# Kernel tuning notes

Measured on AMD Instinct MI355X. Metric: run time of the kernel, lower is better.

The kernel has to match this reference:

```python
import jax, jax.numpy as jnp
import numpy as np

NUM_NODES = 100000
NUM_EDGES = 1600000
NUM_GRAPHS = 1000
NUM_FEATURES = 128
DIM = 32
NUM_CLASSES = 10


def setup_inputs() -> dict:
    key = jax.random.key(0)
    ks = jax.random.split(key, 20)
    inp = {
        "x": jax.random.normal(ks[0], (NUM_NODES, NUM_FEATURES), dtype=jnp.float32),
        "edge_index": jax.random.randint(ks[1], (2, NUM_EDGES), 0, NUM_NODES, dtype=jnp.int64),
        "batch": jnp.sort(jax.random.randint(ks[2], (NUM_NODES,), 0, NUM_GRAPHS, dtype=jnp.int64)),
        "edge_weight": jax.random.uniform(ks[3], (NUM_EDGES,), dtype=jnp.float32),
    }
    # GraphConv params: lin_rel (with bias) on aggregated msgs, lin_root (no bias) on x
    dims = [(NUM_FEATURES, DIM)] + [(DIM, DIM)] * 4
    for i, (fi, fo) in enumerate(dims, start=1):
        s = 1.0 / np.sqrt(fi)
        inp[f"Wrel{i}"] = jax.random.uniform(ks[3 + i], (fi, fo), jnp.float32, -s, s)
        inp[f"brel{i}"] = jax.random.uniform(ks[8 + i], (fo,), jnp.float32, -s, s)
        inp[f"Wroot{i}"] = jax.random.uniform(ks[13 + i], (fi, fo), jnp.float32, -s, s)
    s = 1.0 / np.sqrt(DIM)
    inp["Wlin1"] = jax.random.uniform(ks[19], (DIM, DIM), jnp.float32, -s, s)
    inp["blin1"] = jax.random.uniform(jax.random.fold_in(key, 100), (DIM,), jnp.float32, -s, s)
    inp["Wlin2"] = jax.random.uniform(jax.random.fold_in(key, 101), (DIM, NUM_CLASSES), jnp.float32, -s, s)
    inp["blin2"] = jax.random.uniform(jax.random.fold_in(key, 102), (NUM_CLASSES,), jnp.float32, -s, s)
    return inp


def _graph_conv(x, src, dst, ew, Wrel, brel, Wroot, num_nodes):
    # message: x_j * e_ji ; aggregate (add) at target ; out = lin_rel(agg) + lin_root(x)
    msg = x[src] * ew[:, None]                                   # [E, F_in]
    agg = jax.ops.segment_sum(msg, dst, num_segments=num_nodes)  # [N, F_in]
    return agg @ Wrel + brel + x @ Wroot


def reference(x, edge_index, batch, edge_weight,
              Wrel1, brel1, Wroot1, Wrel2, brel2, Wroot2,
              Wrel3, brel3, Wroot3, Wrel4, brel4, Wroot4,
              Wrel5, brel5, Wroot5, Wlin1, blin1, Wlin2, blin2):
    n = x.shape[0]
    src, dst = edge_index[0], edge_index[1]
    h = jax.nn.relu(_graph_conv(x, src, dst, edge_weight, Wrel1, brel1, Wroot1, n))
    h = jax.nn.relu(_graph_conv(h, src, dst, edge_weight, Wrel2, brel2, Wroot2, n))
    h = jax.nn.relu(_graph_conv(h, src, dst, edge_weight, Wrel3, brel3, Wroot3, n))
    h = jax.nn.relu(_graph_conv(h, src, dst, edge_weight, Wrel4, brel4, Wroot4, n))
    h = jax.nn.relu(_graph_conv(h, src, dst, edge_weight, Wrel5, brel5, Wroot5, n))
    g = jax.ops.segment_sum(h, batch, num_segments=NUM_GRAPHS)   # global_add_pool [G, DIM]
    g = jax.nn.relu(g @ Wlin1 + blin1)
    # dropout p=0.5 is identity in eval mode
    logits = g @ Wlin2 + blin2
    return jax.nn.log_softmax(logits, axis=-1)
```

## Files before the change

kernel.cpp:

```cpp
#include <hip/hip_runtime.h>
#include <stdint.h>

#define NN 100000
#define NE 1600000
#define NG 1000
#define FIN 128
#define DIM 32
#define NC 10

#define NBKT 512
#define NPB 196
#define BCAP 4608
#define RND 2048
#define CURS 16
#define NBINB 782
#define NMM1 1563
#define MM1P1 781
#define MM1P2 782
#define WP 36

typedef unsigned int u32;
typedef __attribute__((ext_vector_type(8))) short short8;
typedef __attribute__((ext_vector_type(4))) float floatx4;
typedef __attribute__((ext_vector_type(4))) unsigned int uint4e;

__device__ __forceinline__ ushort f2bf(float f) {
    u32 b = __float_as_uint(f);
    return (ushort)((b + 0x7FFFu + ((b >> 16) & 1u)) >> 16);
}
__device__ __forceinline__ float bf2f(ushort u) {
    return __uint_as_float(((u32)u) << 16);
}

union SMemU {
    struct {
        uint2  ent[RND];
        ushort bk16[RND];
        int cnt[NBKT]; int sA[NBKT]; int sB[NBKT]; int gbase[NBKT];
    } b;
    struct {
        uint2 ent[BCAP];
        int hist[NPB]; int sc[NPB]; int base[NPB];
    } c;
    struct {
        ushort xs[64 * 136];
        ushort wrel[FIN * WP];
        ushort wroot[FIN * WP];
    } m;
};

__global__ __launch_bounds__(256) void k_init(u32* __restrict__ zp, int zn,
        const float* __restrict__ W1r, const float* __restrict__ W1o,
        const float* __restrict__ W2r, const float* __restrict__ W2o,
        const float* __restrict__ W3r, const float* __restrict__ W3o,
        const float* __restrict__ W4r, const float* __restrict__ W4o,
        ushort* __restrict__ wfrag) {
    int i = blockIdx.x * 256 + threadIdx.x;
    if (i < zn) zp[i] = 0u;
    if (blockIdx.x < 4) {
        const float* Ws[8] = {W1r, W1o, W2r, W2o, W3r, W3o, W4r, W4o};
        int t = threadIdx.x;
        int mat  = t >> 7;
        int nh   = (t >> 6) & 1;
        int lane = t & 63;
        const float* W = Ws[blockIdx.x * 2 + mat];
        int m = lane & 15;
        int g = lane >> 4;
        ushort* dst = wfrag + (((size_t)blockIdx.x * 4 + mat * 2 + nh) * 64 + lane) * 8;
        #pragma unroll
        for (int j = 0; j < 8; ++j)
            dst[j] = f2bf(W[(g * 8 + j) * DIM + nh * 16 + m]);
    }
}

__device__ void bin_body(SMemU& sm, int blk, const int* __restrict__ ei,
        const float* __restrict__ ew, int* __restrict__ cursor,
        uint2* __restrict__ ebuf) {
    int tid = threadIdx.x;
    int e0 = blk * RND;
    int n  = min(RND, NE - e0);

    for (int i = tid; i < NBKT; i += 256) sm.b.cnt[i] = 0;
    __syncthreads();

    u32 pk[8], wv[8], bp[8];
    #pragma unroll
    for (int q = 0; q < 8; ++q) {
        int i = tid + q * 256;
        pk[q] = 0; wv[q] = 0; bp[q] = 0;
        if (i < n) {
            int s = ei[e0 + i];
            int d = ei[NE + e0 + i];
            float w = ew[e0 + i];
            int b = d / NPB;
            int loc = d - b * NPB;
            int p = atomicAdd(&sm.b.cnt[b], 1);
            pk[q] = (u32)s | ((u32)loc << 17);
            wv[q] = __float_as_uint(w);
            bp[q] = (u32)p | ((u32)b << 16);
        }
    }
    __syncthreads();

    for (int i = tid; i < NBKT; i += 256) sm.b.sA[i] = sm.b.cnt[i];
    __syncthreads();
    int* ssrc = sm.b.sA; int* sdst = sm.b.sB;
    for (int dd = 1; dd < NBKT; dd <<= 1) {
        for (int i = tid; i < NBKT; i += 256)
            sdst[i] = ssrc[i] + (i >= dd ? ssrc[i - dd] : 0);
        __syncthreads();
        int* t = ssrc; ssrc = sdst; sdst = t;
    }
    for (int i = tid; i < NBKT; i += 256) {
        int excl = ssrc[i] - sm.b.cnt[i];
        sdst[i] = excl;
        if (sm.b.cnt[i] > 0) sm.b.gbase[i] = atomicAdd(&cursor[i * CURS], sm.b.cnt[i]);
    }
    __syncthreads();
    int* basep = sdst;

    #pragma unroll
    for (int q = 0; q < 8; ++q) {
        int i = tid + q * 256;
        if (i < n) {
            int b = (int)(bp[q] >> 16);
            int p = (int)(bp[q] & 0xFFFFu);
            int pos = basep[b] + p;
            sm.b.ent[pos]  = make_uint2(pk[q], wv[q]);
            sm.b.bk16[pos] = (ushort)b;
        }
    }
    __syncthreads();

    for (int i = tid; i < n; i += 256) {
        int b = (int)sm.b.bk16[i];
        int dsti = sm.b.gbase[b] + (i - basep[b]);
        if (dsti < BCAP) ebuf[(size_t)b * BCAP + dsti] = sm.b.ent[i];
    }
}

__device__ void csr_body(SMemU& sm, int bkt, uint2* __restrict__ ebuf,
        const int* __restrict__ cursor, uint2* __restrict__ od) {
    int tid = threadIdx.x;
    int cnt = min(cursor[bkt * CURS], 4096);
    for (int i = tid; i < NPB; i += 256) sm.c.hist[i] = 0;
    __syncthreads();
    uint2* gb = ebuf + (size_t)bkt * BCAP;
    uint2 my[16]; int mp[16];
    #pragma unroll
    for (int q = 0; q < 16; ++q) {
        int i = tid + q * 256;
        mp[q] = -1;
        if (i < cnt) {
            my[q] = gb[i];
            int loc = (int)(my[q].x >> 17);
            mp[q] = atomicAdd(&sm.c.hist[loc], 1);
        }
    }
    __syncthreads();
    for (int i = tid; i < NPB; i += 256) sm.c.sc[i] = (sm.c.hist[i] + 7) & ~7;
    __syncthreads();
    for (int dd = 1; dd < NPB; dd <<= 1) {
        int v = 0;
        if (tid < NPB) { v = sm.c.sc[tid]; if (tid >= dd) v += sm.c.sc[tid - dd]; }
        __syncthreads();
        if (tid < NPB) sm.c.sc[tid] = v;
        __syncthreads();
    }
    for (int i = tid; i < NPB; i += 256) sm.c.base[i] = sm.c.sc[i] - ((sm.c.hist[i] + 7) & ~7);
    __syncthreads();
    int tot = min(sm.c.sc[NPB - 1], BCAP);
    for (int i = tid; i < tot; i += 256) sm.c.ent[i] = make_uint2(0u, 0u);
    __syncthreads();
    #pragma unroll
    for (int q = 0; q < 16; ++q) {
        if (mp[q] >= 0) {
            int loc = (int)(my[q].x >> 17);
            int pos = sm.c.base[loc] + mp[q];
            if (pos < BCAP) sm.c.ent[pos] = my[q];
        }
    }
    __syncthreads();
    for (int i = tid; i < tot; i += 256) gb[i] = sm.c.ent[i];
    for (int i = tid; i < NPB; i += 256) {
        int node = bkt * NPB + i;
        if (node < NN) {
            int dg = sm.c.hist[i];
            int bs = sm.c.base[i];
            if (bs + ((dg + 7) & ~7) > BCAP) dg = max(0, BCAP - bs) & ~7;
            od[node] = make_uint2((u32)(bkt * BCAP + bs), (u32)dg);
        }
    }
}

__device__ void mm1_body(SMemU& sm, int blk, const float* __restrict__ x,
        const float* __restrict__ Wrel, const float* __restrict__ brel,
        const float* __restrict__ Wroot,
        ushort* __restrict__ ybf, float* __restrict__ aggi) {
    int tid = threadIdx.x;
    int base = blk * 64;
    for (int i = tid; i < FIN * DIM / 4; i += 256) {
        int k = i >> 3, c = i & 7;
        float4 v1 = ((const float4*)Wrel)[i];
        float4 v2 = ((const float4*)Wroot)[i];
        ushort4 u1, u2;
        u1.x = f2bf(v1.x); u1.y = f2bf(v1.y); u1.z = f2bf(v1.z); u1.w = f2bf(v1.w);
        u2.x = f2bf(v2.x); u2.y = f2bf(v2.y); u2.z = f2bf(v2.z); u2.w = f2bf(v2.w);
        *(ushort4*)&sm.m.wrel[k * WP + c * 4]  = u1;
        *(ushort4*)&sm.m.wroot[k * WP + c * 4] = u2;
    }
    for (int i = tid; i < 64 * 32; i += 256) {
        int r = i >> 5, c = i & 31;
        int node = base + r;
        float4 v = make_float4(0.f, 0.f, 0.f, 0.f);
        if (node < NN) v = ((const float4*)x)[(size_t)node * 32 + c];
        ushort4 u;
        u.x = f2bf(v.x); u.y = f2bf(v.y); u.z = f2bf(v.z); u.w = f2bf(v.w);
        *(ushort4*)&sm.m.xs[r * 136 + c * 4] = u;
    }
    __syncthreads();
    int lane = tid & 63;
    int w = tid >> 6;
    int m = lane & 15;
    int q = lane >> 4;
    short8 bfr[4][4];
    #pragma unroll
    for (int nt = 0; nt < 4; ++nt) {
        const ushort* W = (nt < 2) ? sm.m.wrel : sm.m.wroot;
        int ncol = (nt & 1) * 16 + m;
        #pragma unroll
        for (int kc = 0; kc < 4; ++kc) {
            short8 fr;
            #pragma unroll
            for (int j = 0; j < 8; ++j)
                fr[j] = (short)W[(kc * 32 + q * 8 + j) * WP + ncol];
            bfr[nt][kc] = fr;
        }
    }
    floatx4 acc[4] = {{0.f,0.f,0.f,0.f},{0.f,0.f,0.f,0.f},{0.f,0.f,0.f,0.f},{0.f,0.f,0.f,0.f}};
    #pragma unroll
    for (int kc = 0; kc < 4; ++kc) {
        short8 af = *(const short8*)&sm.m.xs[(w * 16 + m) * 136 + kc * 32 + q * 8];
        #pragma unroll
        for (int nt = 0; nt < 4; ++nt)
            acc[nt] = __builtin_amdgcn_mfma_f32_16x16x32_bf16(af, bfr[nt][kc], acc[nt], 0, 0, 0);
    }
    float br0 = brel[m], br1 = brel[16 + m];
    #pragma unroll
    for (int reg = 0; reg < 4; ++reg) {
        int row = q * 4 + reg;
        int node = base + w * 16 + row;
        if (node < NN) {
            ybf[(size_t)node * 32 + m]       = f2bf(acc[0][reg]);
            ybf[(size_t)node * 32 + 16 + m]  = f2bf(acc[1][reg]);
            aggi[(size_t)node * 32 + m]      = acc[2][reg] + br0;
            aggi[(size_t)node * 32 + 16 + m] = acc[3][reg] + br1;
        }
    }
}

__global__ __launch_bounds__(256) void k_pre1(const int* __restrict__ ei,
        const float* __restrict__ ew, int* __restrict__ cursor, uint2* __restrict__ ebuf,
        const float* __restrict__ x, const float* __restrict__ Wrel,
        const float* __restrict__ brel, const float* __restrict__ Wroot,
        ushort* __restrict__ ybf, float* __restrict__ aggi) {
    __shared__ SMemU sm;
    if (blockIdx.x < NBINB) bin_body(sm, blockIdx.x, ei, ew, cursor, ebuf);
    else                    mm1_body(sm, blockIdx.x - NBINB, x, Wrel, brel, Wroot, ybf, aggi);
}

__global__ __launch_bounds__(256) void k_pre2(uint2* __restrict__ ebuf,
        const int* __restrict__ cursor, uint2* __restrict__ od,
        const float* __restrict__ x, const float* __restrict__ Wrel,
        const float* __restrict__ brel, const float* __restrict__ Wroot,
        ushort* __restrict__ ybf, float* __restrict__ aggi) {
    __shared__ SMemU sm;
    if (blockIdx.x < NBKT) csr_body(sm, blockIdx.x, ebuf, cursor, od);
    else                   mm1_body(sm, blockIdx.x - NBKT + MM1P1, x, Wrel, brel, Wroot, ybf, aggi);
}

__device__ __forceinline__ float2 gather_accum(const uint2* __restrict__ eb, int deg,
        const uint* __restrict__ ybp) {
    float acc0 = 0.f, acc1 = 0.f;
    for (int b = 0; b < deg; b += 8) {
        const uint4e* p = (const uint4e*)(eb + b);
        uint4e e0 = __builtin_nontemporal_load(p + 0);
        uint4e e1 = __builtin_nontemporal_load(p + 1);
        uint4e e2 = __builtin_nontemporal_load(p + 2);
        uint4e e3 = __builtin_nontemporal_load(p + 3);
        uint u0 = ybp[(size_t)(e0.x & 0x1FFFFu) * 16];
        uint u1 = ybp[(size_t)(e0.z & 0x1FFFFu) * 16];
        uint u2 = ybp[(size_t)(e1.x & 0x1FFFFu) * 16];
        uint u3 = ybp[(size_t)(e1.z & 0x1FFFFu) * 16];
        uint u4 = ybp[(size_t)(e2.x & 0x1FFFFu) * 16];
        uint u5 = ybp[(size_t)(e2.z & 0x1FFFFu) * 16];
        uint u6 = ybp[(size_t)(e3.x & 0x1FFFFu) * 16];
        uint u7 = ybp[(size_t)(e3.z & 0x1FFFFu) * 16];
        acc0 += __uint_as_float(e0.y) * __uint_as_float(u0 << 16);
        acc1 += __uint_as_float(e0.y) * __uint_as_float(u0 & 0xFFFF0000u);
        acc0 += __uint_as_float(e0.w) * __uint_as_float(u1 << 16);
        acc1 += __uint_as_float(e0.w) * __uint_as_float(u1 & 0xFFFF0000u);
        acc0 += __uint_as_float(e1.y) * __uint_as_float(u2 << 16);
        acc1 += __uint_as_float(e1.y) * __uint_as_float(u2 & 0xFFFF0000u);
        acc0 += __uint_as_float(e1.w) * __uint_as_float(u3 << 16);
        acc1 += __uint_as_float(e1.w) * __uint_as_float(u3 & 0xFFFF0000u);
        acc0 += __uint_as_float(e2.y) * __uint_as_float(u4 << 16);
        acc1 += __uint_as_float(e2.y) * __uint_as_float(u4 & 0xFFFF0000u);
        acc0 += __uint_as_float(e2.w) * __uint_as_float(u5 << 16);
        acc1 += __uint_as_float(e2.w) * __uint_as_float(u5 & 0xFFFF0000u);
        acc0 += __uint_as_float(e3.y) * __uint_as_float(u6 << 16);
        acc1 += __uint_as_float(e3.y) * __uint_as_float(u6 & 0xFFFF0000u);
        acc0 += __uint_as_float(e3.w) * __uint_as_float(u7 << 16);
        acc1 += __uint_as_float(e3.w) * __uint_as_float(u7 & 0xFFFF0000u);
    }
    return make_float2(acc0, acc1);
}

__global__ __launch_bounds__(256, 8) void k_gfused(const ushort* __restrict__ ybf,
        const uint2* __restrict__ ebuf, const uint2* __restrict__ od,
        const float* __restrict__ aggi, const ushort* __restrict__ wfragL,
        const float* __restrict__ brel,
        ushort* __restrict__ ybf_n, float* __restrict__ aggi_n) {
    __shared__ __align__(16) ushort hsm[16 * 40];
    int tid  = threadIdx.x;
    int w    = tid >> 6;
    int lane = tid & 63;
    int nl   = lane >> 4;
    int fp   = lane & 15;
    int node = blockIdx.x * 16 + w * 4 + nl;
    short8 bfr = *(const short8*)&wfragL[((size_t)w * 64 + lane) * 8];
    uint2 o = od[node];
    const uint2* eb = ebuf + o.x;
    const uint* ybp = (const uint*)ybf + fp;
    float2 pv = *(const float2*)&aggi[(size_t)node * DIM + fp * 2];
    float2 ac = gather_accum(eb, (int)o.y, ybp);
    float h0 = fmaxf(pv.x + ac.x, 0.f);
    float h1 = fmaxf(pv.y + ac.y, 0.f);
    u32 hp = (u32)f2bf(h0) | ((u32)f2bf(h1) << 16);
    *(u32*)&hsm[(w * 4 + nl) * 40 + fp * 2] = hp;
    __syncthreads();
    short8 af = *(const short8*)&hsm[(lane & 15) * 40 + (lane >> 4) * 8];
    floatx4 acc = {0.f, 0.f, 0.f, 0.f};
    acc = __builtin_amdgcn_mfma_f32_16x16x32_bf16(af, bfr, acc, 0, 0, 0);
    int ncol  = (w & 1) * 16 + (lane & 15);
    int drow0 = (lane >> 4) * 4;
    size_t obase = ((size_t)blockIdx.x * 16 + drow0) * DIM + ncol;
    if (w < 2) {
        #pragma unroll
        for (int r = 0; r < 4; ++r)
            ybf_n[obase + (size_t)r * DIM] = f2bf(acc[r]);
    } else {
        float bb = brel[ncol];
        #pragma unroll
        for (int r = 0; r < 4; ++r)
            __builtin_nontemporal_store(acc[r] + bb, &aggi_n[obase + (size_t)r * DIM]);
    }
}

__global__ __launch_bounds__(256, 8) void k_glast_pool(const ushort* __restrict__ ybf,
        const uint2* __restrict__ ebuf, const uint2* __restrict__ od,
        const float* __restrict__ aggi, const int* __restrict__ batch,
        float* __restrict__ g) {
    __shared__ __align__(16) float hsm[16][34];
    int tid  = threadIdx.x;
    int w    = tid >> 6;
    int lane = tid & 63;
    int nl   = lane >> 4;
    int fp   = lane & 15;
    int node = blockIdx.x * 16 + w * 4 + nl;
    uint2 o = od[node];
    const uint2* eb = ebuf + o.x;
    const uint* ybp = (const uint*)ybf + fp;
    float2 pv = *(const float2*)&aggi[(size_t)node * DIM + fp * 2];
    float2 ac = gather_accum(eb, (int)o.y, ybp);
    float2 hv;
    hv.x = fmaxf(pv.x + ac.x, 0.f);
    hv.y = fmaxf(pv.y + ac.y, 0.f);
    *(float2*)&hsm[w * 4 + nl][fp * 2] = hv;
    __syncthreads();
    if (tid < 32) {
        int nb = blockIdx.x * 16;
        int curb = batch[nb];
        float run = 0.f;
        #pragma unroll
        for (int n = 0; n < 16; ++n) {
            int b = batch[nb + n];
            if (b != curb) {
                atomicAdd(&g[(size_t)curb * DIM + tid], run);
                run = 0.f; curb = b;
            }
            run += hsm[n][tid];
        }
        atomicAdd(&g[(size_t)curb * DIM + tid], run);
    }
}

__global__ __launch_bounds__(64) void k_head(const float* __restrict__ g,
        const float* __restrict__ W1, const float* __restrict__ b1,
        const float* __restrict__ W2, const float* __restrict__ b2,
        float* __restrict__ out) {
    __shared__ float gs[DIM];
    __shared__ float a1[DIM];
    __shared__ float lg[NC];
    int t = threadIdx.x;
    int gr = blockIdx.x;
    if (t < DIM) gs[t] = g[(size_t)gr * DIM + t];
    __syncthreads();
    if (t < DIM) {
        float a = b1[t];
        #pragma unroll
        for (int k = 0; k < DIM; ++k) a += gs[k] * W1[k * DIM + t];
        a1[t] = fmaxf(a, 0.f);
    }
    __syncthreads();
    if (t < NC) {
        float a = b2[t];
        #pragma unroll
        for (int k = 0; k < DIM; ++k) a += a1[k] * W2[k * NC + t];
        lg[t] = a;
    }
    __syncthreads();
    if (t == 0) {
        float m = lg[0];
        for (int c = 1; c < NC; ++c) m = fmaxf(m, lg[c]);
        float s = 0.f;
        for (int c = 0; c < NC; ++c) s += expf(lg[c] - m);
        float ls = m + logf(s);
        for (int c = 0; c < NC; ++c) out[(size_t)gr * NC + c] = lg[c] - ls;
    }
}

extern "C" void kernel_launch(void* const* d_in, const int* in_sizes, int n_in,
                              void* d_out, int out_size, void* d_ws, size_t ws_size,
                              hipStream_t stream) {
    const float* x     = (const float*)d_in[0];
    const int*   ei    = (const int*)d_in[1];
    const int*   batch = (const int*)d_in[2];
    const float* ew    = (const float*)d_in[3];
    const float* Wrel[5]  = {(const float*)d_in[4],  (const float*)d_in[7],  (const float*)d_in[10], (const float*)d_in[13], (const float*)d_in[16]};
    const float* brel[5]  = {(const float*)d_in[5],  (const float*)d_in[8],  (const float*)d_in[11], (const float*)d_in[14], (const float*)d_in[17]};
    const float* Wroot[5] = {(const float*)d_in[6],  (const float*)d_in[9],  (const float*)d_in[12], (const float*)d_in[15], (const float*)d_in[18]};
    const float* W1 = (const float*)d_in[19];
    const float* b1 = (const float*)d_in[20];
    const float* W2 = (const float*)d_in[21];
    const float* b2 = (const float*)d_in[22];
    float* out = (float*)d_out;

    char* ws = (char*)d_ws;
    const size_t off_cursor = 0;
    const size_t off_g      = 32768;
    const size_t zero_end   = 160768;
    const size_t off_wfrag  = 160768;
    const size_t off_ebuf   = 177152;
    const size_t ebuf_bytes = ((size_t)NBKT * BCAP + 64) * 8;
    const size_t off_od     = off_ebuf + ebuf_bytes;
    const size_t off_A      = off_od + (size_t)NN * 8;
    const size_t off_C      = off_A + (size_t)NN * DIM * 4;
    const size_t off_B1     = off_C + (size_t)NN * DIM * 4;
    const size_t off_B2     = off_B1 + (size_t)NN * DIM * 2;
    const size_t need       = off_B2 + (size_t)NN * DIM * 2;
    if (ws_size < need) return;

    int*    cursor = (int*)(ws + off_cursor);
    float*  g      = (float*)(ws + off_g);
    ushort* wfrag  = (ushort*)(ws + off_wfrag);
    uint2*  ebuf   = (uint2*)(ws + off_ebuf);
    uint2*  od     = (uint2*)(ws + off_od);
    float*  A      = (float*)(ws + off_A);
    float*  C      = (float*)(ws + off_C);
    ushort* B1     = (ushort*)(ws + off_B1);
    ushort* B2     = (ushort*)(ws + off_B2);

    int zcount = (int)(zero_end / 4);
    k_init<<<(zcount + 255) / 256, 256, 0, stream>>>((u32*)ws, zcount,
        Wrel[1], Wroot[1], Wrel[2], Wroot[2], Wrel[3], Wroot[3], Wrel[4], Wroot[4], wfrag);

    k_pre1<<<NBINB + MM1P1, 256, 0, stream>>>(ei, ew, cursor, ebuf,
                                              x, Wrel[0], brel[0], Wroot[0], B1, A);
    k_pre2<<<NBKT + MM1P2, 256, 0, stream>>>(ebuf, cursor, od,
                                             x, Wrel[0], brel[0], Wroot[0], B1, A);

    const int ngt = NN / 16;
    float*  aggc = A;  float*  aggn = C;
    ushort* yc   = B1; ushort* yn   = B2;
    for (int L = 1; L < 5; ++L) {
        k_gfused<<<ngt, 256, 0, stream>>>(yc, ebuf, od, aggc,
                                          wfrag + (size_t)(L - 1) * 2048, brel[L], yn, aggn);
        float* tf = aggc; aggc = aggn; aggn = tf;
        ushort* tu = yc; yc = yn; yn = tu;
    }
    k_glast_pool<<<ngt, 256, 0, stream>>>(yc, ebuf, od, aggc, batch, g);
    k_head<<<NG, 64, 0, stream>>>(g, W1, b1, W2, b2, out);
}
```

Before: 364.3 us.

## Prepack layer-1 weight fragments, use shuffle scans, scatter CSR directly to global

Layer-1 weights are converted to bf16 MFMA fragment layout once in the init kernel, so each mm1 block no longer converts the weights and stages them through shared memory. The bin and CSR prefix scans are replaced with wavefront shuffle scans that need fewer barriers. The CSR step writes entries straight to global memory instead of staging the whole bucket in LDS. Together these shrink shared-memory use per block, which may allow more blocks per CU. The cost is an extra global zero-fill of each bucket plus scattered global writes.

Result: no change. 359.9 us (-1.2%).

```diff
diff --git a/kernel.cpp b/kernel.cpp
--- a/kernel.cpp
+++ b/kernel.cpp
@@ -17,7 +17,6 @@
 #define NMM1 1563
 #define MM1P1 781
 #define MM1P2 782
-#define WP 36
 
 typedef unsigned int u32;
 typedef __attribute__((ext_vector_type(8))) short short8;
@@ -32,62 +31,69 @@
     return __uint_as_float(((u32)u) << 16);
 }
 
-union SMemU {
-    struct {
-        uint2  ent[RND];
-        ushort bk16[RND];
-        int cnt[NBKT]; int sA[NBKT]; int sB[NBKT]; int gbase[NBKT];
-    } b;
-    struct {
-        uint2 ent[BCAP];
-        int hist[NPB]; int sc[NPB]; int base[NPB];
-    } c;
-    struct {
-        ushort xs[64 * 136];
-        ushort wrel[FIN * WP];
-        ushort wroot[FIN * WP];
-    } m;
+struct SBin {
+    uint2  ent[RND];
+    ushort bk16[RND];
+    int cnt[NBKT]; int basep[NBKT]; int gbase[NBKT]; int wsum[4];
 };
+struct SCsr {
+    int hist[NPB]; int base[NPB]; int wsum[4];
+};
+struct SMm {
+    ushort xs[64 * 136];
+};
+union SMem1 { SBin b; SMm m; };
+union SMem2 { SCsr c; SMm m; };
 
 __global__ __launch_bounds__(256) void k_init(u32* __restrict__ zp, int zn,
+        const float* __restrict__ W0r, const float* __restrict__ W0o,
         const float* __restrict__ W1r, const float* __restrict__ W1o,
         const float* __restrict__ W2r, const float* __restrict__ W2o,
         const float* __restrict__ W3r, const float* __restrict__ W3o,
         const float* __restrict__ W4r, const float* __restrict__ W4o,
-        ushort* __restrict__ wfrag) {
+        ushort* __restrict__ wfrag, ushort* __restrict__ wfrag1) {
     int i = blockIdx.x * 256 + threadIdx.x;
     if (i < zn) zp[i] = 0u;
+    int t = threadIdx.x;
+    int mat  = t >> 7;
+    int nh   = (t >> 6) & 1;
+    int lane = t & 63;
+    int m = lane & 15;
+    int g = lane >> 4;
     if (blockIdx.x < 4) {
         const float* Ws[8] = {W1r, W1o, W2r, W2o, W3r, W3o, W4r, W4o};
-        int t = threadIdx.x;
-        int mat  = t >> 7;
-        int nh   = (t >> 6) & 1;
-        int lane = t & 63;
         const float* W = Ws[blockIdx.x * 2 + mat];
-        int m = lane & 15;
-        int g = lane >> 4;
         ushort* dst = wfrag + (((size_t)blockIdx.x * 4 + mat * 2 + nh) * 64 + lane) * 8;
         #pragma unroll
         for (int j = 0; j < 8; ++j)
             dst[j] = f2bf(W[(g * 8 + j) * DIM + nh * 16 + m]);
-    }
-}
-
-__device__ void bin_body(SMemU& sm, int blk, const int* __restrict__ ei,
+    } else if (blockIdx.x < 8) {
+        int kc = blockIdx.x - 4;
+        const float* W = mat ? W0o : W0r;
+        int nt = mat * 2 + nh;
+        ushort* dst = wfrag1 + (((size_t)nt * 4 + kc) * 64 + lane) * 8;
+        #pragma unroll
+        for (int j = 0; j < 8; ++j)
+            dst[j] = f2bf(W[(kc * 32 + g * 8 + j) * DIM + nh * 16 + m]);
+    }
+}
+
+__device__ void bin_body(SMem1& sm, int blk, const int* __restrict__ ei,
         const float* __restrict__ ew, int* __restrict__ cursor,
         uint2* __restrict__ ebuf) {
     int tid = threadIdx.x;
+    int lane = tid & 63, wv = tid >> 6;
     int e0 = blk * RND;
     int n  = min(RND, NE - e0);
 
     for (int i = tid; i < NBKT; i += 256) sm.b.cnt[i] = 0;
     __syncthreads();
 
-    u32 pk[8], wv[8], bp[8];
+    u32 pk[8], wvv[8], bp[8];
     #pragma unroll
     for (int q = 0; q < 8; ++q) {
         int i = tid + q * 256;
-        pk[q] = 0; wv[q] = 0; bp[q] = 0;
+        pk[q] = 0; wvv[q] = 0; bp[q] = 0;
         if (i < n) {
             int s = ei[e0 + i];
             int d = ei[NE + e0 + i];
@@ -96,28 +102,32 @@
             int loc = d - b * NPB;
             int p = atomicAdd(&sm.b.cnt[b], 1);
             pk[q] = (u32)s | ((u32)loc << 17);
-            wv[q] = __float_as_uint(w);
+            wvv[q] = __float_as_uint(w);
             bp[q] = (u32)p | ((u32)b << 16);
         }
     }
     __syncthreads();
 
-    for (int i = tid; i < NBKT; i += 256) sm.b.sA[i] = sm.b.cnt[i];
-    __syncthreads();
-    int* ssrc = sm.b.sA; int* sdst = sm.b.sB;
-    for (int dd = 1; dd < NBKT; dd <<= 1) {
-        for (int i = tid; i < NBKT; i += 256)
-            sdst[i] = ssrc[i] + (i >= dd ? ssrc[i - dd] : 0);
-        __syncthreads();
-        int* t = ssrc; ssrc = sdst; sdst = t;
-    }
-    for (int i = tid; i < NBKT; i += 256) {
-        int excl = ssrc[i] - sm.b.cnt[i];
-        sdst[i] = excl;
+    int a  = sm.b.cnt[2 * tid];
+    int b2 = sm.b.cnt[2 * tid + 1];
+    int s  = a + b2;
+    int inc = s;
+    #pragma unroll
+    for (int d = 1; d < 64; d <<= 1) {
+        int u = __shfl_up(inc, d);
+        if (lane >= d) inc += u;
+    }
+    if (lane == 63) sm.b.wsum[wv] = inc;
+    __syncthreads();
+    int off = 0;
+    #pragma unroll
+    for (int w2 = 0; w2 < 3; ++w2) off += (w2 < wv) ? sm.b.wsum[w2] : 0;
+    int ex = off + inc - s;
+    sm.b.basep[2 * tid]     = ex;
+    sm.b.basep[2 * tid + 1] = ex + a;
+    for (int i = tid; i < NBKT; i += 256)
         if (sm.b.cnt[i] > 0) sm.b.gbase[i] = atomicAdd(&cursor[i * CURS], sm.b.cnt[i]);
-    }
-    __syncthreads();
-    int* basep = sdst;
+    __syncthreads();
 
     #pragma unroll
     for (int q = 0; q < 8; ++q) {
@@ -125,8 +135,8 @@
         if (i < n) {
             int b = (int)(bp[q] >> 16);
             int p = (int)(bp[q] & 0xFFFFu);
-            int pos = basep[b] + p;
-            sm.b.ent[pos]  = make_uint2(pk[q], wv[q]);
+            int pos = sm.b.basep[b] + p;
+            sm.b.ent[pos]  = make_uint2(pk[q], wvv[q]);
             sm.b.bk16[pos] = (ushort)b;
         }
     }
@@ -134,14 +144,15 @@
 
     for (int i = tid; i < n; i += 256) {
         int b = (int)sm.b.bk16[i];
-        int dsti = sm.b.gbase[b] + (i - basep[b]);
+        int dsti = sm.b.gbase[b] + (i - sm.b.basep[b]);
         if (dsti < BCAP) ebuf[(size_t)b * BCAP + dsti] = sm.b.ent[i];
     }
 }
 
-__device__ void csr_body(SMemU& sm, int bkt, uint2* __restrict__ ebuf,
+__device__ void csr_body(SMem2& sm, int bkt, uint2* __restrict__ ebuf,
         const int* __restrict__ cursor, uint2* __restrict__ od) {
     int tid = threadIdx.x;
+    int lane = tid & 63, wvx = tid >> 6;
     int cnt = min(cursor[bkt * CURS], 4096);
     for (int i = tid; i < NPB; i += 256) sm.c.hist[i] = 0;
     __syncthreads();
@@ -158,30 +169,33 @@
         }
     }
     __syncthreads();
-    for (int i = tid; i < NPB; i += 256) sm.c.sc[i] = (sm.c.hist[i] + 7) & ~7;
-    __syncthreads();
-    for (int dd = 1; dd < NPB; dd <<= 1) {
-        int v = 0;
-        if (tid < NPB) { v = sm.c.sc[tid]; if (tid >= dd) v += sm.c.sc[tid - dd]; }
-        __syncthreads();
-        if (tid < NPB) sm.c.sc[tid] = v;
-        __syncthreads();
-    }
-    for (int i = tid; i < NPB; i += 256) sm.c.base[i] = sm.c.sc[i] - ((sm.c.hist[i] + 7) & ~7);
-    __syncthreads();
-    int tot = min(sm.c.sc[NPB - 1], BCAP);
-    for (int i = tid; i < tot; i += 256) sm.c.ent[i] = make_uint2(0u, 0u);
+    int h  = (tid < NPB) ? sm.c.hist[tid] : 0;
+    int hp = (h + 7) & ~7;
+    int inc = hp;
+    #pragma unroll
+    for (int d = 1; d < 64; d <<= 1) {
+        int u = __shfl_up(inc, d);
+        if (lane >= d) inc += u;
+    }
+    if (lane == 63) sm.c.wsum[wvx] = inc;
+    __syncthreads();
+    int off = 0;
+    #pragma unroll
+    for (int w2 = 0; w2 < 3; ++w2) off += (w2 < wvx) ? sm.c.wsum[w2] : 0;
+    if (tid < NPB) sm.c.base[tid] = off + inc - hp;
+    __syncthreads();
+    int tot = sm.c.wsum[0] + sm.c.wsum[1] + sm.c.wsum[2] + sm.c.wsum[3];
+    tot = min(tot, BCAP);
+    for (int i = tid; i < tot; i += 256) gb[i] = make_uint2(0u, 0u);
     __syncthreads();
     #pragma unroll
     for (int q = 0; q < 16; ++q) {
         if (mp[q] >= 0) {
             int loc = (int)(my[q].x >> 17);
             int pos = sm.c.base[loc] + mp[q];
-            if (pos < BCAP) sm.c.ent[pos] = my[q];
-        }
-    }
-    __syncthreads();
-    for (int i = tid; i < tot; i += 256) gb[i] = sm.c.ent[i];
+            if (pos < BCAP) gb[pos] = my[q];
+        }
+    }
     for (int i = tid; i < NPB; i += 256) {
         int node = bkt * NPB + i;
         if (node < NN) {
@@ -193,22 +207,11 @@
     }
 }
 
-__device__ void mm1_body(SMemU& sm, int blk, const float* __restrict__ x,
-        const float* __restrict__ Wrel, const float* __restrict__ brel,
-        const float* __restrict__ Wroot,
+__device__ void mm1_body(ushort* __restrict__ xs, int blk, const float* __restrict__ x,
+        const ushort* __restrict__ wfrag1, const float* __restrict__ brel,
         ushort* __restrict__ ybf, float* __restrict__ aggi) {
     int tid = threadIdx.x;
     int base = blk * 64;
-    for (int i = tid; i < FIN * DIM / 4; i += 256) {
-        int k = i >> 3, c = i & 7;
-        float4 v1 = ((const float4*)Wrel)[i];
-        float4 v2 = ((const float4*)Wroot)[i];
-        ushort4 u1, u2;
-        u1.x = f2bf(v1.x); u1.y = f2bf(v1.y); u1.z = f2bf(v1.z); u1.w = f2bf(v1.w);
-        u2.x = f2bf(v2.x); u2.y = f2bf(v2.y); u2.z = f2bf(v2.z); u2.w = f2bf(v2.w);
-        *(ushort4*)&sm.m.wrel[k * WP + c * 4]  = u1;
-        *(ushort4*)&sm.m.wroot[k * WP + c * 4] = u2;
-    }
     for (int i = tid; i < 64 * 32; i += 256) {
         int r = i >> 5, c = i & 31;
         int node = base + r;
@@ -216,31 +219,23 @@
         if (node < NN) v = ((const float4*)x)[(size_t)node * 32 + c];
         ushort4 u;
         u.x = f2bf(v.x); u.y = f2bf(v.y); u.z = f2bf(v.z); u.w = f2bf(v.w);
-        *(ushort4*)&sm.m.xs[r * 136 + c * 4] = u;
-    }
-    __syncthreads();
+        *(ushort4*)&xs[r * 136 + c * 4] = u;
+    }
     int lane = tid & 63;
     int w = tid >> 6;
     int m = lane & 15;
     int q = lane >> 4;
     short8 bfr[4][4];
     #pragma unroll
-    for (int nt = 0; nt < 4; ++nt) {
-        const ushort* W = (nt < 2) ? sm.m.wrel : sm.m.wroot;
-        int ncol = (nt & 1) * 16 + m;
-        #pragma unroll
-        for (int kc = 0; kc < 4; ++kc) {
-            short8 fr;
-            #pragma unroll
-            for (int j = 0; j < 8; ++j)
-                fr[j] = (short)W[(kc * 32 + q * 8 + j) * WP + ncol];
-            bfr[nt][kc] = fr;
-        }
-    }
+    for (int nt = 0; nt < 4; ++nt)
+        #pragma unroll
+        for (int kc = 0; kc < 4; ++kc)
+            bfr[nt][kc] = *(const short8*)&wfrag1[(((size_t)nt * 4 + kc) * 64 + lane) * 8];
+    __syncthreads();
     floatx4 acc[4] = {{0.f,0.f,0.f,0.f},{0.f,0.f,0.f,0.f},{0.f,0.f,0.f,0.f},{0.f,0.f,0.f,0.f}};
     #pragma unroll
     for (int kc = 0; kc < 4; ++kc) {
-        short8 af = *(const short8*)&sm.m.xs[(w * 16 + m) * 136 + kc * 32 + q * 8];
+        short8 af = *(const short8*)&xs[(w * 16 + m) * 136 + kc * 32 + q * 8];
         #pragma unroll
         for (int nt = 0; nt < 4; ++nt)
             acc[nt] = __builtin_amdgcn_mfma_f32_16x16x32_bf16(af, bfr[nt][kc], acc[nt], 0, 0, 0);
@@ -261,22 +256,22 @@
 
 __global__ __launch_bounds__(256) void k_pre1(const int* __restrict__ ei,
         const float* __restrict__ ew, int* __restrict__ cursor, uint2* __restrict__ ebuf,
-        const float* __restrict__ x, const float* __restrict__ Wrel,
-        const float* __restrict__ brel, const float* __restrict__ Wroot,
+        const float* __restrict__ x, const ushort* __restrict__ wfrag1,
+        const float* __restrict__ brel,
         ushort* __restrict__ ybf, float* __restrict__ aggi) {
-    __shared__ SMemU sm;
+    __shared__ SMem1 sm;
     if (blockIdx.x < NBINB) bin_body(sm, blockIdx.x, ei, ew, cursor, ebuf);
-    else                    mm1_body(sm, blockIdx.x - NBINB, x, Wrel, brel, Wroot, ybf, aggi);
+    else                    mm1_body(sm.m.xs, blockIdx.x - NBINB, x, wfrag1, brel, ybf, aggi);
 }
 
 __global__ __launch_bounds__(256) void k_pre2(uint2* __restrict__ ebuf,
         const int* __restrict__ cursor, uint2* __restrict__ od,
-        const float* __restrict__ x, const float* __restrict__ Wrel,
-        const float* __restrict__ brel, const float* __restrict__ Wroot,
+        const float* __restrict__ x, const ushort* __restrict__ wfrag1,
+        const float* __restrict__ brel,
         ushort* __restrict__ ybf, float* __restrict__ aggi) {
-    __shared__ SMemU sm;
+    __shared__ SMem2 sm;
     if (blockIdx.x < NBKT) csr_body(sm, blockIdx.x, ebuf, cursor, od);
-    else                   mm1_body(sm, blockIdx.x - NBKT + MM1P1, x, Wrel, brel, Wroot, ybf, aggi);
+    else                   mm1_body(sm.m.xs, blockIdx.x - NBKT + MM1P1, x, wfrag1, brel, ybf, aggi);
 }
 
 __device__ __forceinline__ float2 gather_accum(const uint2* __restrict__ eb, int deg,
@@ -451,7 +446,8 @@
     const size_t off_g      = 32768;
     const size_t zero_end   = 160768;
     const size_t off_wfrag  = 160768;
-    const size_t off_ebuf   = 177152;
+    const size_t off_wfrag1 = 177152;
+    const size_t off_ebuf   = 193536;
     const size_t ebuf_bytes = ((size_t)NBKT * BCAP + 64) * 8;
     const size_t off_od     = off_ebuf + ebuf_bytes;
     const size_t off_A      = off_od + (size_t)NN * 8;
@@ -464,6 +460,7 @@
     int*    cursor = (int*)(ws + off_cursor);
     float*  g      = (float*)(ws + off_g);
     ushort* wfrag  = (ushort*)(ws + off_wfrag);
+    ushort* wfrag1 = (ushort*)(ws + off_wfrag1);
     uint2*  ebuf   = (uint2*)(ws + off_ebuf);
     uint2*  od     = (uint2*)(ws + off_od);
     float*  A      = (float*)(ws + off_A);
@@ -473,12 +470,13 @@
 
     int zcount = (int)(zero_end / 4);
     k_init<<<(zcount + 255) / 256, 256, 0, stream>>>((u32*)ws, zcount,
-        Wrel[1], Wroot[1], Wrel[2], Wroot[2], Wrel[3], Wroot[3], Wrel[4], Wroot[4], wfrag);
+        Wrel[0], Wroot[0], Wrel[1], Wroot[1], Wrel[2], Wroot[2],
+        Wrel[3], Wroot[3], Wrel[4], Wroot[4], wfrag, wfrag1);
 
     k_pre1<<<NBINB + MM1P1, 256, 0, stream>>>(ei, ew, cursor, ebuf,
-                                              x, Wrel[0], brel[0], Wroot[0], B1, A);
+                                              x, wfrag1, brel[0], B1, A);
     k_pre2<<<NBKT + MM1P2, 256, 0, stream>>>(ebuf, cursor, od,
-                                             x, Wrel[0], brel[0], Wroot[0], B1, A);
+                                             x, wfrag1, brel[0], B1, A);
 
     const int ngt = NN / 16;
     float*  aggc = A;  float*  aggn = C;
```
